# Kernel optimization log

Hardware: AMD Instinct MI355X
Metric: run time of the kernel (lower is better)

The kernel has to match this reference:

```python
import jax, jax.numpy as jnp
import numpy as np

MESSAGE_SIZE = 128
MESSAGE_PASSES = 3
N_BONDS = 7      # Single, Double, Triple, Quadruple, Aromatic, Pi, Universal
N_LAYERS = 8     # 8 bias-free Linear layers, ReLU after the first 7
N_TYPES = 6      # top-4 ranked atoms + atom 0, plus catchall slot (index 5)
ATOM_VALS = [6.0, 7.0, 8.0, 9.0, 16.0, 17.0, 1.0]
TOP_ATOMS = [6.0, 7.0, 8.0, 9.0, 0.0]


def setup_inputs() -> dict:
    key = jax.random.key(0)
    ks = jax.random.split(key, 8)
    B, N, F, D = 128, 128, 75, MESSAGE_SIZE
    g = jax.random.uniform(ks[0], (B, N_BONDS, N, N), dtype=jnp.float32)
    h = jax.random.normal(ks[1], (B, N, F), dtype=jnp.float32)
    # channel 0 carries the atomic number used for GRU routing
    atom_ids = jax.random.randint(ks[2], (B, N), 0, len(ATOM_VALS))
    h = h.at[:, :, 0].set(jnp.asarray(ATOM_VALS, jnp.float32)[atom_ids])
    s = 1.0 / np.sqrt(D)
    msg_W = jax.random.normal(ks[3], (N_BONDS, N_LAYERS, D, D), jnp.float32) * s
    gru_Wih = jax.random.normal(ks[4], (2, N_TYPES, 3 * D, D), jnp.float32) * s  # [regular/universal, type, 3H, H]
    gru_Whh = jax.random.normal(ks[5], (2, N_TYPES, 3 * D, D), jnp.float32) * s
    gru_bih = jax.random.normal(ks[6], (2, N_TYPES, 3 * D), jnp.float32) * s
    gru_bhh = jax.random.normal(ks[7], (2, N_TYPES, 3 * D), jnp.float32) * s
    return dict(g=g, h=h, msg_W=msg_W, gru_Wih=gru_Wih, gru_Whh=gru_Whh,
                gru_bih=gru_bih, gru_bhh=gru_bhh)


def _gru_grouped(x, hx, tid, Wih, Whh, bih, bhh):
    """torch.nn.GRUCell(input=x, hx=hx) with per-node parameter group tid in [0,T).
    Wih/Whh: [T, 3H, H], bih/bhh: [T, 3H]."""
    gx = jnp.einsum('nd,tgd->ntg', x, Wih)   # [n, T, 3H]
    gh = jnp.einsum('nd,tgd->ntg', hx, Whh)
    gx = jnp.take_along_axis(gx, tid[:, None, None], axis=1)[:, 0] + bih[tid]
    gh = jnp.take_along_axis(gh, tid[:, None, None], axis=1)[:, 0] + bhh[tid]
    xr, xz, xn = jnp.split(gx, 3, axis=-1)
    hr, hz, hn = jnp.split(gh, 3, axis=-1)
    r = jax.nn.sigmoid(xr + hr)
    z = jax.nn.sigmoid(xz + hz)
    n = jnp.tanh(xn + r * hn)
    return (1.0 - z) * n + z * hx


def reference(g, h, msg_W, gru_Wih, gru_Whh, gru_bih, gru_bhh):
    B, N, F = h.shape
    D = msg_W.shape[-1]
    h_t = jnp.concatenate([h, jnp.zeros((B, N, D - F), h.dtype)], axis=2)  # [B,N,D]
    atoms = h[:, :, 0].reshape(-1)
    tid = jnp.full(atoms.shape, N_TYPES - 1, jnp.int32)  # default catchall
    for i, a in enumerate(TOP_ATOMS):
        tid = jnp.where(atoms == jnp.float32(a), jnp.int32(i), tid)
    for _ in range(MESSAGE_PASSES):
        # per-bond-type 8-layer bias-free MLP, vectorized over the 7 bond types
        xb = jnp.broadcast_to(h_t[None], (N_BONDS, B, N, D))
        for l in range(N_LAYERS):
            xb = jnp.einsum('kbnd,ked->kbne', xb, msg_W[:, l])
            if l < N_LAYERS - 1:
                xb = jax.nn.relu(xb)
        # bmm aggregation per bond type: m_k = g[:,k] @ xb_k
        m_all = jnp.einsum('bknm,kbmd->kbnd', g, xb)
        m_non = m_all[:N_BONDS - 1].sum(0).reshape(-1, D)
        m_uni = m_all[N_BONDS - 1].reshape(-1, D)
        h_flat = h_t.reshape(-1, D)
        out = _gru_grouped(h_flat, m_non, tid, gru_Wih[0], gru_Whh[0], gru_bih[0], gru_bhh[0])
        out_u = _gru_grouped(h_flat, m_uni, tid, gru_Wih[1], gru_Whh[1], gru_bih[1], gru_bhh[1])
        h_t = (out + out_u).reshape(B, N, D)
    return h_t
```

## Files before the change

### kernel.cpp

```cpp
#include <hip/hip_runtime.h>
#include <math.h>

#define NBOND 7
#define NLAY 8
#define NTYPE 6
#define NNODES 16384
#define PX 136
#define NDESC 520

typedef _Float16 half8 __attribute__((ext_vector_type(8)));
typedef _Float16 half4 __attribute__((ext_vector_type(4)));
typedef float floatx16 __attribute__((ext_vector_type(16)));

__device__ __forceinline__ float sig_(float x) { return 1.0f / (1.0f + __expf(-x)); }
__device__ __forceinline__ int drow_(int reg, int hi) { return (reg & 3) + 8 * (reg >> 2) + 4 * hi; }

__device__ __forceinline__ _Float16 hi_(float v) { return (_Float16)v; }
__device__ __forceinline__ _Float16 lo_(float v) { return (_Float16)(v - (float)(_Float16)v); }

__global__ void setup_kernel(const float* __restrict__ h, float* __restrict__ hT,
                             int* __restrict__ counts, int* __restrict__ bucket)
{
    int gid = blockIdx.x * 256 + threadIdx.x;
    int node = gid >> 7, d = gid & 127;
    hT[gid] = (d < 75) ? h[node * 75 + d] : 0.0f;
    if (gid < NNODES) {
        float a = h[gid * 75];
        int tt = 5;
        if      (a == 6.0f) tt = 0;
        else if (a == 7.0f) tt = 1;
        else if (a == 8.0f) tt = 2;
        else if (a == 9.0f) tt = 3;
        else if (a == 0.0f) tt = 4;
        int slot = atomicAdd(&counts[tt], 1);
        bucket[tt * NNODES + slot] = gid;
    }
}

__global__ void build_desc_kernel(const int* __restrict__ counts, int* __restrict__ desc)
{
    if (threadIdx.x != 0 || blockIdx.x != 0) return;
    int i = 0;
    for (int tt = 0; tt < NTYPE; ++tt) {
        int nb = (counts[tt] + 31) >> 5;
        for (int s = 0; s < nb; ++s) desc[i++] = tt | (s << 3);
    }
    while (i < NDESC) desc[i++] = -1;
}

__global__ void pack_msg_kernel(const float* __restrict__ msgW, _Float16* __restrict__ Wp)
{
    int idx = blockIdx.x * 256 + threadIdx.x;
    if (idx >= NBOND * NLAY * 16 * 128) return;
    int e  = idx & 127;
    int c  = (idx >> 7) & 15;
    int kl = idx >> 11;
    const float* src = msgW + ((size_t)kl * 128 + e) * 128 + c * 8;
    float4 u = *(const float4*)src;
    float4 v = *(const float4*)(src + 4);
    float av[8] = {u.x, u.y, u.z, u.w, v.x, v.y, v.z, v.w};
    half8 hh, ll;
    #pragma unroll
    for (int j = 0; j < 8; ++j) { hh[j] = hi_(av[j]); ll[j] = lo_(av[j]); }
    _Float16* dst = Wp + ((size_t)kl * 16 + c) * 2048;
    *(half8*)(dst + e * 8)        = hh;
    *(half8*)(dst + 1024 + e * 8) = ll;
}

__global__ void pack_gru_kernel(const float* __restrict__ Wih, const float* __restrict__ Whh,
                                _Float16* __restrict__ Wp)
{
    int idx = blockIdx.x * 256 + threadIdx.x;
    if (idx >= 2 * NTYPE * 2 * 16 * 384) return;
    int col = idx % 384;
    int c   = (idx / 384) & 15;
    int vm  = idx / 6144;
    int mat = vm & 1;
    int vt  = vm >> 1;
    const float* src = (mat ? Whh : Wih) + ((size_t)vt * 384 + col) * 128 + c * 8;
    float4 u = *(const float4*)src;
    float4 v = *(const float4*)(src + 4);
    float av[8] = {u.x, u.y, u.z, u.w, v.x, v.y, v.z, v.w};
    half8 hh, ll;
    #pragma unroll
    for (int j = 0; j < 8; ++j) { hh[j] = hi_(av[j]); ll[j] = lo_(av[j]); }
    _Float16* dst = Wp + (size_t)vm * 98304 + (size_t)c * 6144;
    *(half8*)(dst + col * 8)        = hh;
    *(half8*)(dst + 3072 + col * 8) = ll;
}

__global__ __launch_bounds__(512, 4) void mlp_agg_mfma(
    const float* __restrict__ hin, const _Float16* __restrict__ Wp,
    const float* __restrict__ gmat, float* __restrict__ m_non, float* __restrict__ m_uni)
{
    __shared__ _Float16 Xhi[128 * PX];
    __shared__ _Float16 Xlo[128 * PX];

    const int t = threadIdx.x;
    const int kb = blockIdx.x, b = blockIdx.y;
    const int wave = t >> 6, lane = t & 63, lo = lane & 31, hi = lane >> 5;
    const int ctw = wave & 3, rh = wave >> 2;
    const int wcol = ctw * 32 + lo;

    for (int q = t; q < 128 * 32; q += 512) {
        int r = q >> 5, c4 = q & 31;
        float4 v = *(const float4*)(hin + ((size_t)(b * 128 + r)) * 128 + c4 * 4);
        half4 hh, ll;
        hh[0] = hi_(v.x); ll[0] = lo_(v.x);
        hh[1] = hi_(v.y); ll[1] = lo_(v.y);
        hh[2] = hi_(v.z); ll[2] = lo_(v.z);
        hh[3] = hi_(v.w); ll[3] = lo_(v.w);
        *(half4*)(Xhi + r * PX + c4 * 4) = hh;
        *(half4*)(Xlo + r * PX + c4 * 4) = ll;
    }
    __syncthreads();

    floatx16 acc[2];

    #pragma unroll 1
    for (int l = 0; l < NLAY; ++l) {
        #pragma unroll
        for (int r2 = 0; r2 < 2; ++r2) acc[r2] = (floatx16)0.0f;
        const _Float16* wb = Wp + ((size_t)(kb * NLAY + l) * 16) * 2048;

        #pragma unroll
        for (int kk = 0; kk < 8; ++kk) {
            const _Float16* bp = wb + (size_t)(kk * 2 + hi) * 2048;
            half8 b_h = *(const half8*)(bp + wcol * 8);
            half8 b_l = *(const half8*)(bp + 1024 + wcol * 8);
            #pragma unroll
            for (int r2 = 0; r2 < 2; ++r2) {
                int rrow = (rh * 2 + r2) * 32 + lo;
                half8 a_h = *(const half8*)(Xhi + rrow * PX + kk * 16 + hi * 8);
                half8 a_l = *(const half8*)(Xlo + rrow * PX + kk * 16 + hi * 8);
                acc[r2] = __builtin_amdgcn_mfma_f32_32x32x16_f16(a_h, b_h, acc[r2], 0, 0, 0);
                acc[r2] = __builtin_amdgcn_mfma_f32_32x32x16_f16(a_h, b_l, acc[r2], 0, 0, 0);
                acc[r2] = __builtin_amdgcn_mfma_f32_32x32x16_f16(a_l, b_h, acc[r2], 0, 0, 0);
            }
        }
        __syncthreads();

        if (l < NLAY - 1) {
            #pragma unroll
            for (int r2 = 0; r2 < 2; ++r2)
                #pragma unroll
                for (int reg = 0; reg < 16; ++reg) {
                    int n = (rh * 2 + r2) * 32 + drow_(reg, hi);
                    float vv = fmaxf(acc[r2][reg], 0.0f);
                    Xhi[n * PX + wcol] = hi_(vv);
                    Xlo[n * PX + wcol] = lo_(vv);
                }
        } else {
            #pragma unroll
            for (int r2 = 0; r2 < 2; ++r2)
                #pragma unroll
                for (int s = 0; s < 4; ++s) {
                    int m0 = (rh * 2 + r2) * 32 + 8 * s + 4 * hi;
                    half4 hh, ll;
                    #pragma unroll
                    for (int j = 0; j < 4; ++j) {
                        float vv = acc[r2][4 * s + j];
                        hh[j] = hi_(vv); ll[j] = lo_(vv);
                    }
                    *(half4*)(Xhi + wcol * PX + m0) = hh;
                    *(half4*)(Xlo + wcol * PX + m0) = ll;
                }
        }
        __syncthreads();
    }

    const int rtw = wave & 3, ch = wave >> 2;
    const int row = rtw * 32 + lo;
    #pragma unroll
    for (int c2 = 0; c2 < 2; ++c2) acc[c2] = (floatx16)0.0f;
    const float* grow = gmat + (size_t)(b * NBOND + kb) * 16384;

    #pragma unroll 2
    for (int kk = 0; kk < 8; ++kk) {
        const float* gp = grow + (size_t)row * 128 + kk * 16 + hi * 8;
        float4 u = *(const float4*)gp, v2 = *(const float4*)(gp + 4);
        float av[8] = {u.x, u.y, u.z, u.w, v2.x, v2.y, v2.z, v2.w};
        half8 a_h, a_l;
        #pragma unroll
        for (int j = 0; j < 8; ++j) { a_h[j] = hi_(av[j]); a_l[j] = lo_(av[j]); }
        #pragma unroll
        for (int c2 = 0; c2 < 2; ++c2) {
            int ct = ch * 2 + c2;
            half8 b_h = *(const half8*)(Xhi + (ct * 32 + lo) * PX + kk * 16 + hi * 8);
            half8 b_l = *(const half8*)(Xlo + (ct * 32 + lo) * PX + kk * 16 + hi * 8);
            acc[c2] = __builtin_amdgcn_mfma_f32_32x32x16_f16(a_h, b_h, acc[c2], 0, 0, 0);
            acc[c2] = __builtin_amdgcn_mfma_f32_32x32x16_f16(a_h, b_l, acc[c2], 0, 0, 0);
            acc[c2] = __builtin_amdgcn_mfma_f32_32x32x16_f16(a_l, b_h, acc[c2], 0, 0, 0);
        }
    }

    if (kb == NBOND - 1) {
        #pragma unroll
        for (int c2 = 0; c2 < 2; ++c2)
            #pragma unroll
            for (int reg = 0; reg < 16; ++reg) {
                int n = rtw * 32 + drow_(reg, hi);
                m_uni[((size_t)(b * 128 + n)) * 128 + (ch * 2 + c2) * 32 + lo] = acc[c2][reg];
            }
    } else {
        #pragma unroll
        for (int c2 = 0; c2 < 2; ++c2)
            #pragma unroll
            for (int reg = 0; reg < 16; ++reg) {
                int n = rtw * 32 + drow_(reg, hi);
                atomicAdd(m_non + ((size_t)(b * 128 + n)) * 128 + (ch * 2 + c2) * 32 + lo,
                          acc[c2][reg]);
            }
    }
}

__global__ __launch_bounds__(256, 3) void gru_mfma(
    float* __restrict__ hT,
    const float* __restrict__ m_non, const float* __restrict__ m_uni,
    const int* __restrict__ counts, const int* __restrict__ bucket,
    const int* __restrict__ desc,
    const _Float16* __restrict__ Wp, const float* __restrict__ bihp, const float* __restrict__ bhhp)
{
    __shared__ _Float16 Xh[32 * PX], Xl[32 * PX], Mh[32 * PX], Ml[32 * PX];
    __shared__ int bl[32];

    const int bid = blockIdx.x;
    const int dv = desc[(bid & 7) * (NDESC / 8) + (bid >> 3)];
    if (dv < 0) return;
    const int tt = dv & 7;
    const int base = (dv >> 3) * 32;
    const int t = threadIdx.x;
    const int cnt = counts[tt];
    const int nn = min(32, cnt - base);
    if (t < 32) bl[t] = (t < nn) ? bucket[tt * NNODES + base + t] : -1;
    __syncthreads();

    for (int q = t; q < 32 * 32; q += 256) {
        int r = q >> 5, c4 = q & 31;
        float4 xv = make_float4(0.f, 0.f, 0.f, 0.f);
        int node = bl[r];
        if (node >= 0) xv = *(const float4*)(hT + (size_t)node * 128 + c4 * 4);
        half4 hh, ll;
        hh[0] = hi_(xv.x); ll[0] = lo_(xv.x);
        hh[1] = hi_(xv.y); ll[1] = lo_(xv.y);
        hh[2] = hi_(xv.z); ll[2] = lo_(xv.z);
        hh[3] = hi_(xv.w); ll[3] = lo_(xv.w);
        *(half4*)(Xh + r * PX + c4 * 4) = hh;
        *(half4*)(Xl + r * PX + c4 * 4) = ll;
    }

    const int wave = t >> 6, lane = t & 63, lo = lane & 31, hi = lane >> 5;
    const int d = wave * 32 + lo;

    #pragma unroll 1
    for (int v = 0; v < 2; ++v) {
        const float* msrc = v ? m_uni : m_non;
        __syncthreads();
        for (int q = t; q < 32 * 32; q += 256) {
            int r = q >> 5, c4 = q & 31;
            float4 mv = make_float4(0.f, 0.f, 0.f, 0.f);
            int node = bl[r];
            if (node >= 0) mv = *(const float4*)(msrc + (size_t)node * 128 + c4 * 4);
            half4 hh, ll;
            hh[0] = hi_(mv.x); ll[0] = lo_(mv.x);
            hh[1] = hi_(mv.y); ll[1] = lo_(mv.y);
            hh[2] = hi_(mv.z); ll[2] = lo_(mv.z);
            hh[3] = hi_(mv.w); ll[3] = lo_(mv.w);
            *(half4*)(Mh + r * PX + c4 * 4) = hh;
            *(half4*)(Ml + r * PX + c4 * 4) = ll;
        }
        __syncthreads();

        const int vt = v * NTYPE + tt;
        const _Float16* pih = Wp + (size_t)(vt * 2 + 0) * 98304;
        const _Float16* phh = Wp + (size_t)(vt * 2 + 1) * 98304;

        floatx16 ar = (floatx16)0.0f, az = (floatx16)0.0f;
        floatx16 ax = (floatx16)0.0f, ah = (floatx16)0.0f;

        #pragma unroll 2
        for (int kk = 0; kk < 8; ++kk) {
            int koff = kk * 16 + hi * 8;
            half8 xh = *(const half8*)(Xh + lo * PX + koff);
            half8 xl = *(const half8*)(Xl + lo * PX + koff);
            half8 mh = *(const half8*)(Mh + lo * PX + koff);
            half8 ml = *(const half8*)(Ml + lo * PX + koff);
            const _Float16* ci = pih + (size_t)(kk * 2 + hi) * 6144;
            const _Float16* ch = phh + (size_t)(kk * 2 + hi) * 6144;
            half8 birh = *(const half8*)(ci + (0   + d) * 8);
            half8 birl = *(const half8*)(ci + 3072 + (0   + d) * 8);
            half8 bizh = *(const half8*)(ci + (128 + d) * 8);
            half8 bizl = *(const half8*)(ci + 3072 + (128 + d) * 8);
            half8 binh = *(const half8*)(ci + (256 + d) * 8);
            half8 binl = *(const half8*)(ci + 3072 + (256 + d) * 8);
            half8 bhrh = *(const half8*)(ch + (0   + d) * 8);
            half8 bhrl = *(const half8*)(ch + 3072 + (0   + d) * 8);
            half8 bhzh = *(const half8*)(ch + (128 + d) * 8);
            half8 bhzl = *(const half8*)(ch + 3072 + (128 + d) * 8);
            half8 bhnh = *(const half8*)(ch + (256 + d) * 8);
            half8 bhnl = *(const half8*)(ch + 3072 + (256 + d) * 8);

            ar = __builtin_amdgcn_mfma_f32_32x32x16_f16(xh, birh, ar, 0, 0, 0);
            ar = __builtin_amdgcn_mfma_f32_32x32x16_f16(xh, birl, ar, 0, 0, 0);
            ar = __builtin_amdgcn_mfma_f32_32x32x16_f16(xl, birh, ar, 0, 0, 0);
            ar = __builtin_amdgcn_mfma_f32_32x32x16_f16(mh, bhrh, ar, 0, 0, 0);
            ar = __builtin_amdgcn_mfma_f32_32x32x16_f16(mh, bhrl, ar, 0, 0, 0);
            ar = __builtin_amdgcn_mfma_f32_32x32x16_f16(ml, bhrh, ar, 0, 0, 0);

            az = __builtin_amdgcn_mfma_f32_32x32x16_f16(xh, bizh, az, 0, 0, 0);
            az = __builtin_amdgcn_mfma_f32_32x32x16_f16(xh, bizl, az, 0, 0, 0);
            az = __builtin_amdgcn_mfma_f32_32x32x16_f16(xl, bizh, az, 0, 0, 0);
            az = __builtin_amdgcn_mfma_f32_32x32x16_f16(mh, bhzh, az, 0, 0, 0);
            az = __builtin_amdgcn_mfma_f32_32x32x16_f16(mh, bhzl, az, 0, 0, 0);
            az = __builtin_amdgcn_mfma_f32_32x32x16_f16(ml, bhzh, az, 0, 0, 0);

            ax = __builtin_amdgcn_mfma_f32_32x32x16_f16(xh, binh, ax, 0, 0, 0);
            ax = __builtin_amdgcn_mfma_f32_32x32x16_f16(xh, binl, ax, 0, 0, 0);
            ax = __builtin_amdgcn_mfma_f32_32x32x16_f16(xl, binh, ax, 0, 0, 0);
            ah = __builtin_amdgcn_mfma_f32_32x32x16_f16(mh, bhnh, ah, 0, 0, 0);
            ah = __builtin_amdgcn_mfma_f32_32x32x16_f16(mh, bhnl, ah, 0, 0, 0);
            ah = __builtin_amdgcn_mfma_f32_32x32x16_f16(ml, bhnh, ah, 0, 0, 0);
        }

        const float* bi = bihp + (size_t)vt * 384;
        const float* bh = bhhp + (size_t)vt * 384;
        float b_r  = bi[d] + bh[d];
        float b_z  = bi[128 + d] + bh[128 + d];
        float b_in = bi[256 + d];
        float b_hn = bh[256 + d];
        #pragma unroll
        for (int reg = 0; reg < 16; ++reg) {
            int n = drow_(reg, hi);
            int node = bl[n];
            if (node < 0) continue;
            float r  = sig_(ar[reg] + b_r);
            float z  = sig_(az[reg] + b_z);
            float nv = tanhf(ax[reg] + b_in + r * (ah[reg] + b_hn));
            float mv = msrc[(size_t)node * 128 + d];
            float val = (1.0f - z) * nv + z * mv;
            if (v == 0) hT[(size_t)node * 128 + d] = val;
            else        hT[(size_t)node * 128 + d] += val;
        }
    }
}

extern "C" void kernel_launch(void* const* d_in, const int* in_sizes, int n_in,
                              void* d_out, int out_size, void* d_ws, size_t ws_size,
                              hipStream_t stream) {
    const float* g    = (const float*)d_in[0];
    const float* h    = (const float*)d_in[1];
    const float* msgW = (const float*)d_in[2];
    const float* Wih  = (const float*)d_in[3];
    const float* Whh  = (const float*)d_in[4];
    const float* bih  = (const float*)d_in[5];
    const float* bhh  = (const float*)d_in[6];
    float* hT = (float*)d_out;

    char* ws = (char*)d_ws;
    float* m_non = (float*)ws;
    float* m_uni = m_non + (size_t)NNODES * 128;
    int* counts  = (int*)(ws + 2 * (size_t)NNODES * 128 * 4);
    int* bucket  = counts + 8;
    int* desc    = bucket + NTYPE * NNODES;
    _Float16* WpM = (_Float16*)(desc + NDESC);
    _Float16* WpG = WpM + (size_t)NBOND * NLAY * 16 * 2048;

    (void)hipMemsetAsync(counts, 0, 8 * sizeof(int), stream);
    setup_kernel<<<NNODES * 128 / 256, 256, 0, stream>>>(h, hT, counts, bucket);
    build_desc_kernel<<<1, 64, 0, stream>>>(counts, desc);
    pack_msg_kernel<<<(NBOND * NLAY * 16 * 128 + 255) / 256, 256, 0, stream>>>(msgW, WpM);
    pack_gru_kernel<<<(2 * NTYPE * 2 * 16 * 384 + 255) / 256, 256, 0, stream>>>(Wih, Whh, WpG);

    for (int pass = 0; pass < 3; ++pass) {
        (void)hipMemsetAsync(m_non, 0, (size_t)NNODES * 128 * 4, stream);
        mlp_agg_mfma<<<dim3(NBOND, 128), 512, 0, stream>>>(hT, WpM, g, m_non, m_uni);
        gru_mfma<<<dim3(NDESC), 256, 0, stream>>>(hT, m_non, m_uni, counts, bucket, desc,
                                                  WpG, bih, bhh);
    }
}
```

Before: 782.1 us.

## Double GRU node tile to 64 rows and remap MLP grid for XCD locality

The GRU kernel now processes 64 nodes per block instead of 32, so each loaded weight fragment feeds two MFMA row tiles. This halves global weight traffic per node and the block count, at the cost of more registers and LDS, and lowers the launch-bounds occupancy target from 3 to 2. The MLP kernel moves to a 1D grid with a swizzled block-to-(bond, batch) mapping, so that blocks sharing a bond type's weights tend to land on the same XCD and share its L2.

```diff
diff --git a/kernel.cpp b/kernel.cpp
--- a/kernel.cpp
+++ b/kernel.cpp
@@ -6,7 +6,7 @@
 #define NTYPE 6
 #define NNODES 16384
 #define PX 136
-#define NDESC 520
+#define NDESC 264
 
 typedef _Float16 half8 __attribute__((ext_vector_type(8)));
 typedef _Float16 half4 __attribute__((ext_vector_type(4)));
@@ -42,7 +42,7 @@
     if (threadIdx.x != 0 || blockIdx.x != 0) return;
     int i = 0;
     for (int tt = 0; tt < NTYPE; ++tt) {
-        int nb = (counts[tt] + 31) >> 5;
+        int nb = (counts[tt] + 63) >> 6;
         for (int s = 0; s < nb; ++s) desc[i++] = tt | (s << 3);
     }
     while (i < NDESC) desc[i++] = -1;
@@ -96,8 +96,10 @@
     __shared__ _Float16 Xhi[128 * PX];
     __shared__ _Float16 Xlo[128 * PX];
 
+    const int bid = blockIdx.x;
+    const int w12 = (bid & 7) * 112 + (bid >> 3);
+    const int kb = w12 >> 7, b = w12 & 127;
     const int t = threadIdx.x;
-    const int kb = blockIdx.x, b = blockIdx.y;
     const int wave = t >> 6, lane = t & 63, lo = lane & 31, hi = lane >> 5;
     const int ctw = wave & 3, rh = wave >> 2;
     const int wcol = ctw * 32 + lo;
@@ -214,28 +216,28 @@
     }
 }
 
-__global__ __launch_bounds__(256, 3) void gru_mfma(
+__global__ __launch_bounds__(256, 2) void gru_mfma(
     float* __restrict__ hT,
     const float* __restrict__ m_non, const float* __restrict__ m_uni,
     const int* __restrict__ counts, const int* __restrict__ bucket,
     const int* __restrict__ desc,
     const _Float16* __restrict__ Wp, const float* __restrict__ bihp, const float* __restrict__ bhhp)
 {
-    __shared__ _Float16 Xh[32 * PX], Xl[32 * PX], Mh[32 * PX], Ml[32 * PX];
-    __shared__ int bl[32];
+    __shared__ _Float16 Xh[64 * PX], Xl[64 * PX], Mh[64 * PX], Ml[64 * PX];
+    __shared__ int bl[64];
 
     const int bid = blockIdx.x;
     const int dv = desc[(bid & 7) * (NDESC / 8) + (bid >> 3)];
     if (dv < 0) return;
     const int tt = dv & 7;
-    const int base = (dv >> 3) * 32;
+    const int base = (dv >> 3) * 64;
     const int t = threadIdx.x;
     const int cnt = counts[tt];
-    const int nn = min(32, cnt - base);
-    if (t < 32) bl[t] = (t < nn) ? bucket[tt * NNODES + base + t] : -1;
+    const int nn = min(64, cnt - base);
+    if (t < 64) bl[t] = (t < nn) ? bucket[tt * NNODES + base + t] : -1;
     __syncthreads();
 
-    for (int q = t; q < 32 * 32; q += 256) {
+    for (int q = t; q < 64 * 32; q += 256) {
         int r = q >> 5, c4 = q & 31;
         float4 xv = make_float4(0.f, 0.f, 0.f, 0.f);
         int node = bl[r];
@@ -256,7 +258,7 @@
     for (int v = 0; v < 2; ++v) {
         const float* msrc = v ? m_uni : m_non;
         __syncthreads();
-        for (int q = t; q < 32 * 32; q += 256) {
+        for (int q = t; q < 64 * 32; q += 256) {
             int r = q >> 5, c4 = q & 31;
             float4 mv = make_float4(0.f, 0.f, 0.f, 0.f);
             int node = bl[r];
@@ -275,51 +277,88 @@
         const _Float16* pih = Wp + (size_t)(vt * 2 + 0) * 98304;
         const _Float16* phh = Wp + (size_t)(vt * 2 + 1) * 98304;
 
-        floatx16 ar = (floatx16)0.0f, az = (floatx16)0.0f;
-        floatx16 ax = (floatx16)0.0f, ah = (floatx16)0.0f;
+        floatx16 ar[2], az[2], ax[2], ah[2];
+        #pragma unroll
+        for (int r2 = 0; r2 < 2; ++r2) {
+            ar[r2] = (floatx16)0.0f; az[r2] = (floatx16)0.0f;
+            ax[r2] = (floatx16)0.0f; ah[r2] = (floatx16)0.0f;
+        }
 
         #pragma unroll 2
         for (int kk = 0; kk < 8; ++kk) {
             int koff = kk * 16 + hi * 8;
-            half8 xh = *(const half8*)(Xh + lo * PX + koff);
-            half8 xl = *(const half8*)(Xl + lo * PX + koff);
-            half8 mh = *(const half8*)(Mh + lo * PX + koff);
-            half8 ml = *(const half8*)(Ml + lo * PX + koff);
+            half8 xh[2], xl[2], mh[2], ml[2];
+            #pragma unroll
+            for (int r2 = 0; r2 < 2; ++r2) {
+                int rr = r2 * 32 + lo;
+                xh[r2] = *(const half8*)(Xh + rr * PX + koff);
+                xl[r2] = *(const half8*)(Xl + rr * PX + koff);
+                mh[r2] = *(const half8*)(Mh + rr * PX + koff);
+                ml[r2] = *(const half8*)(Ml + rr * PX + koff);
+            }
             const _Float16* ci = pih + (size_t)(kk * 2 + hi) * 6144;
             const _Float16* ch = phh + (size_t)(kk * 2 + hi) * 6144;
-            half8 birh = *(const half8*)(ci + (0   + d) * 8);
-            half8 birl = *(const half8*)(ci + 3072 + (0   + d) * 8);
-            half8 bizh = *(const half8*)(ci + (128 + d) * 8);
-            half8 bizl = *(const half8*)(ci + 3072 + (128 + d) * 8);
-            half8 binh = *(const half8*)(ci + (256 + d) * 8);
-            half8 binl = *(const half8*)(ci + 3072 + (256 + d) * 8);
-            half8 bhrh = *(const half8*)(ch + (0   + d) * 8);
-            half8 bhrl = *(const half8*)(ch + 3072 + (0   + d) * 8);
-            half8 bhzh = *(const half8*)(ch + (128 + d) * 8);
-            half8 bhzl = *(const half8*)(ch + 3072 + (128 + d) * 8);
-            half8 bhnh = *(const half8*)(ch + (256 + d) * 8);
-            half8 bhnl = *(const half8*)(ch + 3072 + (256 + d) * 8);
-
-            ar = __builtin_amdgcn_mfma_f32_32x32x16_f16(xh, birh, ar, 0, 0, 0);
-            ar = __builtin_amdgcn_mfma_f32_32x32x16_f16(xh, birl, ar, 0, 0, 0);
-            ar = __builtin_amdgcn_mfma_f32_32x32x16_f16(xl, birh, ar, 0, 0, 0);
-            ar = __builtin_amdgcn_mfma_f32_32x32x16_f16(mh, bhrh, ar, 0, 0, 0);
-            ar = __builtin_amdgcn_mfma_f32_32x32x16_f16(mh, bhrl, ar, 0, 0, 0);
-            ar = __builtin_amdgcn_mfma_f32_32x32x16_f16(ml, bhrh, ar, 0, 0, 0);
-
-            az = __builtin_amdgcn_mfma_f32_32x32x16_f16(xh, bizh, az, 0, 0, 0);
-            az = __builtin_amdgcn_mfma_f32_32x32x16_f16(xh, bizl, az, 0, 0, 0);
-            az = __builtin_amdgcn_mfma_f32_32x32x16_f16(xl, bizh, az, 0, 0, 0);
-            az = __builtin_amdgcn_mfma_f32_32x32x16_f16(mh, bhzh, az, 0, 0, 0);
-            az = __builtin_amdgcn_mfma_f32_32x32x16_f16(mh, bhzl, az, 0, 0, 0);
-            az = __builtin_amdgcn_mfma_f32_32x32x16_f16(ml, bhzh, az, 0, 0, 0);
-
-            ax = __builtin_amdgcn_mfma_f32_32x32x16_f16(xh, binh, ax, 0, 0, 0);
-            ax = __builtin_amdgcn_mfma_f32_32x32x16_f16(xh, binl, ax, 0, 0, 0);
-            ax = __builtin_amdgcn_mfma_f32_32x32x16_f16(xl, binh, ax, 0, 0, 0);
-            ah = __builtin_amdgcn_mfma_f32_32x32x16_f16(mh, bhnh, ah, 0, 0, 0);
-            ah = __builtin_amdgcn_mfma_f32_32x32x16_f16(mh, bhnl, ah, 0, 0, 0);
-            ah = __builtin_amdgcn_mfma_f32_32x32x16_f16(ml, bhnh, ah, 0, 0, 0);
+
+            {
+                half8 wh = *(const half8*)(ci + (0 + d) * 8);
+                half8 wl = *(const half8*)(ci + 3072 + (0 + d) * 8);
+                #pragma unroll
+                for (int r2 = 0; r2 < 2; ++r2) {
+                    ar[r2] = __builtin_amdgcn_mfma_f32_32x32x16_f16(xh[r2], wh, ar[r2], 0, 0, 0);
+                    ar[r2] = __builtin_amdgcn_mfma_f32_32x32x16_f16(xh[r2], wl, ar[r2], 0, 0, 0);
+                    ar[r2] = __builtin_amdgcn_mfma_f32_32x32x16_f16(xl[r2], wh, ar[r2], 0, 0, 0);
+                }
+            }
+            {
+                half8 wh = *(const half8*)(ch + (0 + d) * 8);
+                half8 wl = *(const half8*)(ch + 3072 + (0 + d) * 8);
+                #pragma unroll
+                for (int r2 = 0; r2 < 2; ++r2) {
+                    ar[r2] = __builtin_amdgcn_mfma_f32_32x32x16_f16(mh[r2], wh, ar[r2], 0, 0, 0);
+                    ar[r2] = __builtin_amdgcn_mfma_f32_32x32x16_f16(mh[r2], wl, ar[r2], 0, 0, 0);
+                    ar[r2] = __builtin_amdgcn_mfma_f32_32x32x16_f16(ml[r2], wh, ar[r2], 0, 0, 0);
+                }
+            }
+            {
+                half8 wh = *(const half8*)(ci + (128 + d) * 8);
+                half8 wl = *(const half8*)(ci + 3072 + (128 + d) * 8);
+                #pragma unroll
+                for (int r2 = 0; r2 < 2; ++r2) {
+                    az[r2] = __builtin_amdgcn_mfma_f32_32x32x16_f16(xh[r2], wh, az[r2], 0, 0, 0);
+                    az[r2] = __builtin_amdgcn_mfma_f32_32x32x16_f16(xh[r2], wl, az[r2], 0, 0, 0);
+                    az[r2] = __builtin_amdgcn_mfma_f32_32x32x16_f16(xl[r2], wh, az[r2], 0, 0, 0);
+                }
+            }
+            {
+                half8 wh = *(const half8*)(ch + (128 + d) * 8);
+                half8 wl = *(const half8*)(ch + 3072 + (128 + d) * 8);
+                #pragma unroll
+                for (int r2 = 0; r2 < 2; ++r2) {
+                    az[r2] = __builtin_amdgcn_mfma_f32_32x32x16_f16(mh[r2], wh, az[r2], 0, 0, 0);
+                    az[r2] = __builtin_amdgcn_mfma_f32_32x32x16_f16(mh[r2], wl, az[r2], 0, 0, 0);
+                    az[r2] = __builtin_amdgcn_mfma_f32_32x32x16_f16(ml[r2], wh, az[r2], 0, 0, 0);
+                }
+            }
+            {
+                half8 wh = *(const half8*)(ci + (256 + d) * 8);
+                half8 wl = *(const half8*)(ci + 3072 + (256 + d) * 8);
+                #pragma unroll
+                for (int r2 = 0; r2 < 2; ++r2) {
+                    ax[r2] = __builtin_amdgcn_mfma_f32_32x32x16_f16(xh[r2], wh, ax[r2], 0, 0, 0);
+                    ax[r2] = __builtin_amdgcn_mfma_f32_32x32x16_f16(xh[r2], wl, ax[r2], 0, 0, 0);
+                    ax[r2] = __builtin_amdgcn_mfma_f32_32x32x16_f16(xl[r2], wh, ax[r2], 0, 0, 0);
+                }
+            }
+            {
+                half8 wh = *(const half8*)(ch + (256 + d) * 8);
+                half8 wl = *(const half8*)(ch + 3072 + (256 + d) * 8);
+                #pragma unroll
+                for (int r2 = 0; r2 < 2; ++r2) {
+                    ah[r2] = __builtin_amdgcn_mfma_f32_32x32x16_f16(mh[r2], wh, ah[r2], 0, 0, 0);
+                    ah[r2] = __builtin_amdgcn_mfma_f32_32x32x16_f16(mh[r2], wl, ah[r2], 0, 0, 0);
+                    ah[r2] = __builtin_amdgcn_mfma_f32_32x32x16_f16(ml[r2], wh, ah[r2], 0, 0, 0);
+                }
+            }
         }
 
         const float* bi = bihp + (size_t)vt * 384;
@@ -329,18 +368,20 @@
         float b_in = bi[256 + d];
         float b_hn = bh[256 + d];
         #pragma unroll
-        for (int reg = 0; reg < 16; ++reg) {
-            int n = drow_(reg, hi);
-            int node = bl[n];
-            if (node < 0) continue;
-            float r  = sig_(ar[reg] + b_r);
-            float z  = sig_(az[reg] + b_z);
-            float nv = tanhf(ax[reg] + b_in + r * (ah[reg] + b_hn));
-            float mv = msrc[(size_t)node * 128 + d];
-            float val = (1.0f - z) * nv + z * mv;
-            if (v == 0) hT[(size_t)node * 128 + d] = val;
-            else        hT[(size_t)node * 128 + d] += val;
-        }
+        for (int r2 = 0; r2 < 2; ++r2)
+            #pragma unroll
+            for (int reg = 0; reg < 16; ++reg) {
+                int n = r2 * 32 + drow_(reg, hi);
+                int node = bl[n];
+                if (node < 0) continue;
+                float r  = sig_(ar[r2][reg] + b_r);
+                float z  = sig_(az[r2][reg] + b_z);
+                float nv = tanhf(ax[r2][reg] + b_in + r * (ah[r2][reg] + b_hn));
+                float mv = msrc[(size_t)node * 128 + d];
+                float val = (1.0f - z) * nv + z * mv;
+                if (v == 0) hT[(size_t)node * 128 + d] = val;
+                else        hT[(size_t)node * 128 + d] += val;
+            }
     }
 }
 
@@ -373,7 +414,7 @@
 
     for (int pass = 0; pass < 3; ++pass) {
         (void)hipMemsetAsync(m_non, 0, (size_t)NNODES * 128 * 4, stream);
-        mlp_agg_mfma<<<dim3(NBOND, 128), 512, 0, stream>>>(hT, WpM, g, m_non, m_uni);
+        mlp_agg_mfma<<<dim3(NBOND * 128), 512, 0, stream>>>(hT, WpM, g, m_non, m_uni);
         gru_mfma<<<dim3(NDESC), 256, 0, stream>>>(hT, m_non, m_uni, counts, bucket, desc,
                                                   WpG, bih, bhh);
     }
```

New measurement: 822.9 us. 5.2% more time.

## Prefetch next layer's weights into registers during MFMA loop in MLP kernel

Applied to the files above, without the earlier changes.

Loads all 16 half8 weight fragments for a layer into registers up front with inline-asm global loads, and issues the next layer's loads right after the current layer's MFMAs so they overlap the ReLU write-back and barriers. Replaces __syncthreads with raw s_barrier plus explicit waitcnt, and lowers the occupancy hint in launch_bounds from 4 to 2 blocks to leave room for the extra registers. This hides global weight-load latency but raises register pressure and relies on hand-managed vmcnt waits being correct.

```diff
diff --git a/kernel.cpp b/kernel.cpp
--- a/kernel.cpp
+++ b/kernel.cpp
@@ -17,6 +17,13 @@
 
 __device__ __forceinline__ _Float16 hi_(float v) { return (_Float16)v; }
 __device__ __forceinline__ _Float16 lo_(float v) { return (_Float16)(v - (float)(_Float16)v); }
+
+__device__ __forceinline__ void ldg128(half8& d, const _Float16* p) {
+    asm volatile("global_load_dwordx4 %0, %1, off" : "=v"(d) : "v"(p) : "memory");
+}
+__device__ __forceinline__ void ldg128_o2048(half8& d, const _Float16* p) {
+    asm volatile("global_load_dwordx4 %0, %1, off offset:2048" : "=v"(d) : "v"(p) : "memory");
+}
 
 __global__ void setup_kernel(const float* __restrict__ h, float* __restrict__ hT,
                              int* __restrict__ counts, int* __restrict__ bucket)
@@ -89,7 +96,7 @@
     *(half8*)(dst + 3072 + col * 8) = ll;
 }
 
-__global__ __launch_bounds__(512, 4) void mlp_agg_mfma(
+__global__ __launch_bounds__(512, 2) void mlp_agg_mfma(
     const float* __restrict__ hin, const _Float16* __restrict__ Wp,
     const float* __restrict__ gmat, float* __restrict__ m_non, float* __restrict__ m_uni)
 {
@@ -101,6 +108,18 @@
     const int wave = t >> 6, lane = t & 63, lo = lane & 31, hi = lane >> 5;
     const int ctw = wave & 3, rh = wave >> 2;
     const int wcol = ctw * 32 + lo;
+
+    half8 Wh[8], Wl[8];
+
+    {
+        const _Float16* wb0 = Wp + ((size_t)(kb * NLAY) * 16) * 2048;
+        #pragma unroll
+        for (int kk = 0; kk < 8; ++kk) {
+            const _Float16* bp = wb0 + (size_t)(kk * 2 + hi) * 2048 + wcol * 8;
+            ldg128(Wh[kk], bp);
+            ldg128_o2048(Wl[kk], bp);
+        }
+    }
 
     for (int q = t; q < 128 * 32; q += 512) {
         int r = q >> 5, c4 = q & 31;
@@ -119,26 +138,38 @@
 
     #pragma unroll 1
     for (int l = 0; l < NLAY; ++l) {
+        asm volatile("s_waitcnt vmcnt(0)" ::: "memory");
+        __builtin_amdgcn_sched_barrier(0);
+
         #pragma unroll
         for (int r2 = 0; r2 < 2; ++r2) acc[r2] = (floatx16)0.0f;
-        const _Float16* wb = Wp + ((size_t)(kb * NLAY + l) * 16) * 2048;
 
         #pragma unroll
         for (int kk = 0; kk < 8; ++kk) {
-            const _Float16* bp = wb + (size_t)(kk * 2 + hi) * 2048;
-            half8 b_h = *(const half8*)(bp + wcol * 8);
-            half8 b_l = *(const half8*)(bp + 1024 + wcol * 8);
             #pragma unroll
             for (int r2 = 0; r2 < 2; ++r2) {
                 int rrow = (rh * 2 + r2) * 32 + lo;
                 half8 a_h = *(const half8*)(Xhi + rrow * PX + kk * 16 + hi * 8);
                 half8 a_l = *(const half8*)(Xlo + rrow * PX + kk * 16 + hi * 8);
-                acc[r2] = __builtin_amdgcn_mfma_f32_32x32x16_f16(a_h, b_h, acc[r2], 0, 0, 0);
-                acc[r2] = __builtin_amdgcn_mfma_f32_32x32x16_f16(a_h, b_l, acc[r2], 0, 0, 0);
-                acc[r2] = __builtin_amdgcn_mfma_f32_32x32x16_f16(a_l, b_h, acc[r2], 0, 0, 0);
+                acc[r2] = __builtin_amdgcn_mfma_f32_32x32x16_f16(a_h, Wh[kk], acc[r2], 0, 0, 0);
+                acc[r2] = __builtin_amdgcn_mfma_f32_32x32x16_f16(a_h, Wl[kk], acc[r2], 0, 0, 0);
+                acc[r2] = __builtin_amdgcn_mfma_f32_32x32x16_f16(a_l, Wh[kk], acc[r2], 0, 0, 0);
             }
         }
-        __syncthreads();
+
+        if (l < NLAY - 1) {
+            const _Float16* wbn = Wp + ((size_t)(kb * NLAY + l + 1) * 16) * 2048;
+            #pragma unroll
+            for (int kk = 0; kk < 8; ++kk) {
+                const _Float16* bp = wbn + (size_t)(kk * 2 + hi) * 2048 + wcol * 8;
+                ldg128(Wh[kk], bp);
+                ldg128_o2048(Wl[kk], bp);
+            }
+        }
+        __builtin_amdgcn_sched_barrier(0);
+
+        asm volatile("" ::: "memory");
+        __builtin_amdgcn_s_barrier();
 
         if (l < NLAY - 1) {
             #pragma unroll
@@ -166,7 +197,10 @@
                     *(half4*)(Xlo + wcol * PX + m0) = ll;
                 }
         }
-        __syncthreads();
+
+        asm volatile("s_waitcnt lgkmcnt(0)" ::: "memory");
+        __builtin_amdgcn_s_barrier();
+        asm volatile("" ::: "memory");
     }
 
     const int rtw = wave & 3, ch = wave >> 2;
```

After: 855.7 us. 9.4% more time.

## Split MLP-aggregation blocks by node half and accumulate partial bmm via atomics

Applied to the files above, without the earlier changes.

Each MLP+aggregation block now handles 64 nodes of one graph instead of 128, using 256 threads and half the shared memory, so twice as many smaller blocks launch and occupancy goes up. Because the aggregation sums over all 128 nodes, each half-block computes a partial product over its 64 source nodes and atomically adds it into both m_non and m_uni. m_uni is therefore zeroed as well, and the grid is reordered so the node index varies fastest. The cost is twice as many global atomics, and the transposed tile uses a 68-element stride that needs split 64-bit LDS loads.

```diff
diff --git a/kernel.cpp b/kernel.cpp
--- a/kernel.cpp
+++ b/kernel.cpp
@@ -6,6 +6,7 @@
 #define NTYPE 6
 #define NNODES 16384
 #define PX 136
+#define PXT 68
 #define NDESC 520
 
 typedef _Float16 half8 __attribute__((ext_vector_type(8)));
@@ -17,6 +18,13 @@
 
 __device__ __forceinline__ _Float16 hi_(float v) { return (_Float16)v; }
 __device__ __forceinline__ _Float16 lo_(float v) { return (_Float16)(v - (float)(_Float16)v); }
+
+__device__ __forceinline__ half8 ld_h8_2x64(const _Float16* p) {
+    half4 a = *(const half4*)p;
+    half4 b = *(const half4*)(p + 4);
+    half8 r = {a[0], a[1], a[2], a[3], b[0], b[1], b[2], b[3]};
+    return r;
+}
 
 __global__ void setup_kernel(const float* __restrict__ h, float* __restrict__ hT,
                              int* __restrict__ counts, int* __restrict__ bucket)
@@ -89,22 +97,22 @@
     *(half8*)(dst + 3072 + col * 8) = ll;
 }
 
-__global__ __launch_bounds__(512, 4) void mlp_agg_mfma(
+__global__ __launch_bounds__(256, 4) void mlp_agg_mfma(
     const float* __restrict__ hin, const _Float16* __restrict__ Wp,
     const float* __restrict__ gmat, float* __restrict__ m_non, float* __restrict__ m_uni)
 {
-    __shared__ _Float16 Xhi[128 * PX];
-    __shared__ _Float16 Xlo[128 * PX];
-
+    __shared__ _Float16 Xhi[64 * PX];
+    __shared__ _Float16 Xlo[64 * PX];
+
+    const int nb = blockIdx.x, kb = blockIdx.y;
+    const int b = nb >> 1, mh = nb & 1;
     const int t = threadIdx.x;
-    const int kb = blockIdx.x, b = blockIdx.y;
     const int wave = t >> 6, lane = t & 63, lo = lane & 31, hi = lane >> 5;
-    const int ctw = wave & 3, rh = wave >> 2;
-    const int wcol = ctw * 32 + lo;
-
-    for (int q = t; q < 128 * 32; q += 512) {
+    const int wcol = wave * 32 + lo;
+
+    for (int q = t; q < 64 * 32; q += 256) {
         int r = q >> 5, c4 = q & 31;
-        float4 v = *(const float4*)(hin + ((size_t)(b * 128 + r)) * 128 + c4 * 4);
+        float4 v = *(const float4*)(hin + ((size_t)(nb * 64 + r)) * 128 + c4 * 4);
         half4 hh, ll;
         hh[0] = hi_(v.x); ll[0] = lo_(v.x);
         hh[1] = hi_(v.y); ll[1] = lo_(v.y);
@@ -130,7 +138,7 @@
             half8 b_l = *(const half8*)(bp + 1024 + wcol * 8);
             #pragma unroll
             for (int r2 = 0; r2 < 2; ++r2) {
-                int rrow = (rh * 2 + r2) * 32 + lo;
+                int rrow = r2 * 32 + lo;
                 half8 a_h = *(const half8*)(Xhi + rrow * PX + kk * 16 + hi * 8);
                 half8 a_l = *(const half8*)(Xlo + rrow * PX + kk * 16 + hi * 8);
                 acc[r2] = __builtin_amdgcn_mfma_f32_32x32x16_f16(a_h, b_h, acc[r2], 0, 0, 0);
@@ -145,7 +153,7 @@
             for (int r2 = 0; r2 < 2; ++r2)
                 #pragma unroll
                 for (int reg = 0; reg < 16; ++reg) {
-                    int n = (rh * 2 + r2) * 32 + drow_(reg, hi);
+                    int n = r2 * 32 + drow_(reg, hi);
                     float vv = fmaxf(acc[r2][reg], 0.0f);
                     Xhi[n * PX + wcol] = hi_(vv);
                     Xlo[n * PX + wcol] = lo_(vv);
@@ -155,63 +163,52 @@
             for (int r2 = 0; r2 < 2; ++r2)
                 #pragma unroll
                 for (int s = 0; s < 4; ++s) {
-                    int m0 = (rh * 2 + r2) * 32 + 8 * s + 4 * hi;
+                    int m0 = r2 * 32 + 8 * s + 4 * hi;
                     half4 hh, ll;
                     #pragma unroll
                     for (int j = 0; j < 4; ++j) {
                         float vv = acc[r2][4 * s + j];
                         hh[j] = hi_(vv); ll[j] = lo_(vv);
                     }
-                    *(half4*)(Xhi + wcol * PX + m0) = hh;
-                    *(half4*)(Xlo + wcol * PX + m0) = ll;
+                    *(half4*)(Xhi + wcol * PXT + m0) = hh;
+                    *(half4*)(Xlo + wcol * PXT + m0) = ll;
                 }
         }
         __syncthreads();
     }
 
-    const int rtw = wave & 3, ch = wave >> 2;
-    const int row = rtw * 32 + lo;
-    #pragma unroll
-    for (int c2 = 0; c2 < 2; ++c2) acc[c2] = (floatx16)0.0f;
+    floatx16 agg[4];
+    #pragma unroll
+    for (int ct = 0; ct < 4; ++ct) agg[ct] = (floatx16)0.0f;
     const float* grow = gmat + (size_t)(b * NBOND + kb) * 16384;
-
-    #pragma unroll 2
-    for (int kk = 0; kk < 8; ++kk) {
-        const float* gp = grow + (size_t)row * 128 + kk * 16 + hi * 8;
+    const int row = wave * 32 + lo;
+
+    #pragma unroll
+    for (int kk = 0; kk < 4; ++kk) {
+        const float* gp = grow + (size_t)row * 128 + mh * 64 + kk * 16 + hi * 8;
         float4 u = *(const float4*)gp, v2 = *(const float4*)(gp + 4);
         float av[8] = {u.x, u.y, u.z, u.w, v2.x, v2.y, v2.z, v2.w};
         half8 a_h, a_l;
         #pragma unroll
         for (int j = 0; j < 8; ++j) { a_h[j] = hi_(av[j]); a_l[j] = lo_(av[j]); }
         #pragma unroll
-        for (int c2 = 0; c2 < 2; ++c2) {
-            int ct = ch * 2 + c2;
-            half8 b_h = *(const half8*)(Xhi + (ct * 32 + lo) * PX + kk * 16 + hi * 8);
-            half8 b_l = *(const half8*)(Xlo + (ct * 32 + lo) * PX + kk * 16 + hi * 8);
-            acc[c2] = __builtin_amdgcn_mfma_f32_32x32x16_f16(a_h, b_h, acc[c2], 0, 0, 0);
-            acc[c2] = __builtin_amdgcn_mfma_f32_32x32x16_f16(a_h, b_l, acc[c2], 0, 0, 0);
-            acc[c2] = __builtin_amdgcn_mfma_f32_32x32x16_f16(a_l, b_h, acc[c2], 0, 0, 0);
-        }
-    }
-
-    if (kb == NBOND - 1) {
-        #pragma unroll
-        for (int c2 = 0; c2 < 2; ++c2)
-            #pragma unroll
-            for (int reg = 0; reg < 16; ++reg) {
-                int n = rtw * 32 + drow_(reg, hi);
-                m_uni[((size_t)(b * 128 + n)) * 128 + (ch * 2 + c2) * 32 + lo] = acc[c2][reg];
-            }
-    } else {
-        #pragma unroll
-        for (int c2 = 0; c2 < 2; ++c2)
-            #pragma unroll
-            for (int reg = 0; reg < 16; ++reg) {
-                int n = rtw * 32 + drow_(reg, hi);
-                atomicAdd(m_non + ((size_t)(b * 128 + n)) * 128 + (ch * 2 + c2) * 32 + lo,
-                          acc[c2][reg]);
-            }
-    }
+        for (int ct = 0; ct < 4; ++ct) {
+            half8 b_h = ld_h8_2x64(Xhi + (ct * 32 + lo) * PXT + kk * 16 + hi * 8);
+            half8 b_l = ld_h8_2x64(Xlo + (ct * 32 + lo) * PXT + kk * 16 + hi * 8);
+            agg[ct] = __builtin_amdgcn_mfma_f32_32x32x16_f16(a_h, b_h, agg[ct], 0, 0, 0);
+            agg[ct] = __builtin_amdgcn_mfma_f32_32x32x16_f16(a_h, b_l, agg[ct], 0, 0, 0);
+            agg[ct] = __builtin_amdgcn_mfma_f32_32x32x16_f16(a_l, b_h, agg[ct], 0, 0, 0);
+        }
+    }
+
+    float* mdst = (kb == NBOND - 1) ? m_uni : m_non;
+    #pragma unroll
+    for (int ct = 0; ct < 4; ++ct)
+        #pragma unroll
+        for (int reg = 0; reg < 16; ++reg) {
+            int n = wave * 32 + drow_(reg, hi);
+            atomicAdd(mdst + ((size_t)(b * 128 + n)) * 128 + ct * 32 + lo, agg[ct][reg]);
+        }
 }
 
 __global__ __launch_bounds__(256, 3) void gru_mfma(
@@ -372,8 +369,8 @@
     pack_gru_kernel<<<(2 * NTYPE * 2 * 16 * 384 + 255) / 256, 256, 0, stream>>>(Wih, Whh, WpG);
 
     for (int pass = 0; pass < 3; ++pass) {
-        (void)hipMemsetAsync(m_non, 0, (size_t)NNODES * 128 * 4, stream);
-        mlp_agg_mfma<<<dim3(NBOND, 128), 512, 0, stream>>>(hT, WpM, g, m_non, m_uni);
+        (void)hipMemsetAsync(m_non, 0, 2 * (size_t)NNODES * 128 * 4, stream);
+        mlp_agg_mfma<<<dim3(256, NBOND), 256, 0, stream>>>(hT, WpM, g, m_non, m_uni);
         gru_mfma<<<dim3(NDESC), 256, 0, stream>>>(hT, m_non, m_uni, counts, bucket, desc,
                                                   WpG, bih, bhh);
     }
```

Result: slower. 832.3 us (+6.4%).
